# Optimization experiments

Hardware: AMD Instinct MI355X
Metric: run time of the kernel (lower is better)

Reference implementation:

```python
import jax, jax.numpy as jnp
import numpy as np

ENC_DIM, DEC_DIM, JOINT_DIM, VOCAB = 512, 640, 512, 1024
B, T, U = 8, 256, 64


def setup_inputs() -> dict:
    key = jax.random.key(0)
    ks = jax.random.split(key, 8)
    s_enc = 1.0 / np.sqrt(ENC_DIM)
    s_dec = 1.0 / np.sqrt(DEC_DIM)
    s_out = 1.0 / np.sqrt(2 * JOINT_DIM)
    return {
        "enc_out": jax.random.normal(ks[0], (B, T, ENC_DIM), jnp.float32),
        "pred_out": jax.random.normal(ks[1], (B, U, DEC_DIM), jnp.float32),
        "W_enc": jax.random.uniform(ks[2], (JOINT_DIM, ENC_DIM), jnp.float32, -s_enc, s_enc),
        "b_enc": jax.random.uniform(ks[3], (JOINT_DIM,), jnp.float32, -s_enc, s_enc),
        "W_pred": jax.random.uniform(ks[4], (JOINT_DIM, DEC_DIM), jnp.float32, -s_dec, s_dec),
        "b_pred": jax.random.uniform(ks[5], (JOINT_DIM,), jnp.float32, -s_dec, s_dec),
        "W_out": jax.random.uniform(ks[6], (VOCAB, 2 * JOINT_DIM), jnp.float32, -s_out, s_out),
        "b_out": jax.random.uniform(ks[7], (VOCAB,), jnp.float32, -s_out, s_out),
    }


def reference(enc_out, pred_out, W_enc, b_enc, W_pred, b_pred, W_out, b_out):
    # Dropout is identity in eval mode. fc_out on cat([enc_exp, pred_exp]) is
    # mathematically identical to splitting W_out in half and summing two
    # broadcast projections (avoids materializing the [B,T,U,2J] tensor).
    J = W_enc.shape[0]
    e = jnp.einsum('bte,je->btj', enc_out, W_enc) + b_enc    # [B,T,J]
    p = jnp.einsum('bud,jd->buj', pred_out, W_pred) + b_pred  # [B,U,J]
    W1, W2 = W_out[:, :J], W_out[:, J:]
    out = (jnp.einsum('btj,vj->btv', e, W1)[:, :, None, :]
           + jnp.einsum('buj,vj->buv', p, W2)[:, None, :, :]
           + b_out)                                           # [B,T,U,V]
    return out
```

## Files before the change

### kernel.cpp

```cpp
#include <hip/hip_runtime.h>

typedef float f4 __attribute__((ext_vector_type(4)));
typedef float f32x4 __attribute__((ext_vector_type(4)));
typedef short bf16x8 __attribute__((ext_vector_type(8)));
typedef unsigned short u16x8 __attribute__((ext_vector_type(8)));

static __device__ __forceinline__ unsigned short f2bf(float f) {
    unsigned int x = __builtin_bit_cast(unsigned int, f);
    x = (x + 0x7fffu + ((x >> 16) & 1u)) >> 16;
    return (unsigned short)x;
}
static __device__ __forceinline__ float bf2f(unsigned short h) {
    unsigned int x = ((unsigned int)h) << 16;
    return __builtin_bit_cast(float, x);
}

static __device__ __forceinline__ void gll16(const unsigned short* g, unsigned short* l) {
    __builtin_amdgcn_global_load_lds(
        (__attribute__((address_space(1))) void*)(g),
        (__attribute__((address_space(3))) void*)(l), 16, 0, 0);
}

static __device__ __forceinline__ int fragoff(int r, int s) {
    return r * 32 + ((s ^ ((r >> 1) & 3)) << 3);
}

struct GJobF {
    const float *A, *W;
    int lda, ldw;
    const float* bias;
    unsigned short *Ch, *Cl;
    int N, K, nbx;
};

__global__ __launch_bounds__(256, 3) void gemmcvt64(
    GJobF j0, GJobF j1, int nblk0, int nblk1,
    const float* __restrict__ Wo, unsigned short* __restrict__ Wo_h,
    unsigned short* __restrict__ Wo_l, int nWo8)
{
    __shared__ unsigned short lds[2][4][64 * 32];

    const int bid = blockIdx.x;
    const int tid = threadIdx.x;

    if (bid >= nblk0 + nblk1) {
        const int nblkc = (int)gridDim.x - nblk0 - nblk1;
        for (int g = (bid - nblk0 - nblk1) * 256 + tid; g < nWo8; g += nblkc * 256) {
            const int idx = g * 8;
            f4 a = *(const f4*)(Wo + idx);
            f4 b = *(const f4*)(Wo + idx + 4);
            u16x8 hv, lv;
            float s[8] = { a.x, a.y, a.z, a.w, b.x, b.y, b.z, b.w };
            #pragma unroll
            for (int i = 0; i < 8; ++i) {
                unsigned short h = f2bf(s[i]);
                hv[i] = h;
                lv[i] = f2bf(s[i] - bf2f(h));
            }
            *(u16x8*)(Wo_h + idx) = hv;
            *(u16x8*)(Wo_l + idx) = lv;
        }
        return;
    }

    const bool first = bid < nblk0;
    const GJobF J = first ? j0 : j1;
    const int local = first ? bid : bid - nblk0;
    const int m0 = (local % J.nbx) * 64;
    const int n0 = (local / J.nbx) * 64;

    const int lane = tid & 63;
    const int wid  = tid >> 6;
    const int wr   = wid >> 1, wc = wid & 1;
    const int lrow = lane & 15;
    const int s    = lane >> 4;

    const int row  = tid >> 2, slot = tid & 3;
    const int woff = fragoff(row, slot);
    const float* pA = J.A + (size_t)(m0 + row) * J.lda + slot * 8;
    const float* pW = J.W + (size_t)(n0 + row) * J.ldw + slot * 8;

    f4 ra0, ra1, rw0, rw1;

#define LOADREGS(k0) do { \
    ra0 = *(const f4*)(pA + (k0));     ra1 = *(const f4*)(pA + (k0) + 4); \
    rw0 = *(const f4*)(pW + (k0));     rw1 = *(const f4*)(pW + (k0) + 4); \
} while (0)

#define CVTWRITE(buf) do { \
    u16x8 ha, la, hw, lw; \
    float sa[8] = { ra0.x, ra0.y, ra0.z, ra0.w, ra1.x, ra1.y, ra1.z, ra1.w }; \
    float sw[8] = { rw0.x, rw0.y, rw0.z, rw0.w, rw1.x, rw1.y, rw1.z, rw1.w }; \
    _Pragma("unroll") \
    for (int i = 0; i < 8; ++i) { \
        unsigned short h = f2bf(sa[i]); \
        ha[i] = h; la[i] = f2bf(sa[i] - bf2f(h)); \
        h = f2bf(sw[i]); \
        hw[i] = h; lw[i] = f2bf(sw[i] - bf2f(h)); \
    } \
    *(u16x8*)&lds[buf][0][woff] = ha; \
    *(u16x8*)&lds[buf][1][woff] = la; \
    *(u16x8*)&lds[buf][2][woff] = hw; \
    *(u16x8*)&lds[buf][3][woff] = lw; \
} while (0)

    f32x4 acc[2][2];
    #pragma unroll
    for (int i = 0; i < 2; ++i)
        #pragma unroll
        for (int j = 0; j < 2; ++j) acc[i][j] = (f32x4){0.f, 0.f, 0.f, 0.f};

    const int nt = J.K / 32;

    LOADREGS(0);
    CVTWRITE(0);
    __syncthreads();

    int cur = 0;
    for (int t = 0; t < nt; ++t) {
        if (t + 1 < nt) LOADREGS((t + 1) * 32);

        bf16x8 ah[2], al[2], wh[2], wl[2];
        #pragma unroll
        for (int i = 0; i < 2; ++i) {
            const int ra = wr * 32 + i * 16 + lrow;
            const int rw = wc * 32 + i * 16 + lrow;
            ah[i] = *(const bf16x8*)&lds[cur][0][fragoff(ra, s)];
            al[i] = *(const bf16x8*)&lds[cur][1][fragoff(ra, s)];
            wh[i] = *(const bf16x8*)&lds[cur][2][fragoff(rw, s)];
            wl[i] = *(const bf16x8*)&lds[cur][3][fragoff(rw, s)];
        }
        #pragma unroll
        for (int i = 0; i < 2; ++i)
            #pragma unroll
            for (int j = 0; j < 2; ++j) {
                acc[i][j] = __builtin_amdgcn_mfma_f32_16x16x32_bf16(ah[i], wh[j], acc[i][j], 0, 0, 0);
                acc[i][j] = __builtin_amdgcn_mfma_f32_16x16x32_bf16(ah[i], wl[j], acc[i][j], 0, 0, 0);
                acc[i][j] = __builtin_amdgcn_mfma_f32_16x16x32_bf16(al[i], wh[j], acc[i][j], 0, 0, 0);
            }

        if (t + 1 < nt) {
            CVTWRITE(cur ^ 1);
            __syncthreads();
            cur ^= 1;
        }
    }
#undef LOADREGS
#undef CVTWRITE

    #pragma unroll
    for (int i = 0; i < 2; ++i) {
        const int rbase = m0 + wr * 32 + i * 16 + (lane >> 4) * 4;
        #pragma unroll
        for (int j = 0; j < 2; ++j) {
            const int col = n0 + wc * 32 + j * 16 + (lane & 15);
            const float bv = J.bias[col];
            #pragma unroll
            for (int r = 0; r < 4; ++r) {
                float v = acc[i][j][r] + bv;
                size_t off = (size_t)(rbase + r) * J.N + col;
                unsigned short h = f2bf(v);
                J.Ch[off] = h;
                J.Cl[off] = f2bf(v - bf2f(h));
            }
        }
    }
}

struct GJob {
    const unsigned short *Ah, *Al, *Wh, *Wl;
    int lda, ldw;
    const float* bias;
    float* Cf;
    int N, K, nbx;
};

__global__ __launch_bounds__(256, 3) void gemm64(GJob j0, GJob j1, int nblk0)
{
    __shared__ unsigned short lds[2][4][64 * 32];

    const bool first = (int)blockIdx.x < nblk0;
    const GJob J = first ? j0 : j1;
    const int local = first ? (int)blockIdx.x : (int)blockIdx.x - nblk0;
    const int m0 = (local % J.nbx) * 64;
    const int n0 = (local / J.nbx) * 64;

    const int tid  = threadIdx.x;
    const int lane = tid & 63;
    const int wid  = tid >> 6;
    const int wr   = wid >> 1, wc = wid & 1;
    const int lrow = lane & 15;
    const int s    = lane >> 4;

    const int srow  = wid * 16 + (lane >> 2);
    const int sslot = (lane & 3) ^ ((srow >> 1) & 3);
    const size_t gA = (size_t)(m0 + srow) * J.lda + sslot * 8;
    const size_t gW = (size_t)(n0 + srow) * J.ldw + sslot * 8;

    f32x4 acc[2][2];
    #pragma unroll
    for (int i = 0; i < 2; ++i)
        #pragma unroll
        for (int j = 0; j < 2; ++j) acc[i][j] = (f32x4){0.f, 0.f, 0.f, 0.f};

    const int nt = J.K / 32;

    gll16(J.Ah + gA, &lds[0][0][wid * 512]);
    gll16(J.Al + gA, &lds[0][1][wid * 512]);
    gll16(J.Wh + gW, &lds[0][2][wid * 512]);
    gll16(J.Wl + gW, &lds[0][3][wid * 512]);
    asm volatile("s_waitcnt vmcnt(0)" ::: "memory");
    __syncthreads();

    int cur = 0;
    for (int t = 0; t < nt; ++t) {
        if (t + 1 < nt) {
            const int k0 = (t + 1) * 32;
            gll16(J.Ah + gA + k0, &lds[cur ^ 1][0][wid * 512]);
            gll16(J.Al + gA + k0, &lds[cur ^ 1][1][wid * 512]);
            gll16(J.Wh + gW + k0, &lds[cur ^ 1][2][wid * 512]);
            gll16(J.Wl + gW + k0, &lds[cur ^ 1][3][wid * 512]);
        }

        bf16x8 ah[2], al[2], wh[2], wl[2];
        #pragma unroll
        for (int i = 0; i < 2; ++i) {
            const int ra = wr * 32 + i * 16 + lrow;
            const int rw = wc * 32 + i * 16 + lrow;
            ah[i] = *(const bf16x8*)&lds[cur][0][fragoff(ra, s)];
            al[i] = *(const bf16x8*)&lds[cur][1][fragoff(ra, s)];
            wh[i] = *(const bf16x8*)&lds[cur][2][fragoff(rw, s)];
            wl[i] = *(const bf16x8*)&lds[cur][3][fragoff(rw, s)];
        }
        #pragma unroll
        for (int i = 0; i < 2; ++i)
            #pragma unroll
            for (int j = 0; j < 2; ++j) {
                acc[i][j] = __builtin_amdgcn_mfma_f32_16x16x32_bf16(ah[i], wh[j], acc[i][j], 0, 0, 0);
                acc[i][j] = __builtin_amdgcn_mfma_f32_16x16x32_bf16(ah[i], wl[j], acc[i][j], 0, 0, 0);
                acc[i][j] = __builtin_amdgcn_mfma_f32_16x16x32_bf16(al[i], wh[j], acc[i][j], 0, 0, 0);
            }

        if (t + 1 < nt) {
            asm volatile("s_waitcnt vmcnt(0)" ::: "memory");
            __syncthreads();
            cur ^= 1;
        }
    }

    #pragma unroll
    for (int i = 0; i < 2; ++i) {
        const int rbase = m0 + wr * 32 + i * 16 + (lane >> 4) * 4;
        #pragma unroll
        for (int j = 0; j < 2; ++j) {
            const int col = n0 + wc * 32 + j * 16 + (lane & 15);
            const float bv = J.bias ? J.bias[col] : 0.f;
            #pragma unroll
            for (int r = 0; r < 4; ++r)
                J.Cf[(size_t)(rbase + r) * J.N + col] = acc[i][j][r] + bv;
        }
    }
}

__global__ __launch_bounds__(256) void bcast_kernel(
    const float* __restrict__ X, const float* __restrict__ Y,
    float* __restrict__ out, int T, int U)
{
    const int Vq  = 256;
    const int bt  = blockIdx.x;
    const int b   = bt / T;
    const int tid = threadIdx.x;

    const f4* X4 = (const f4*)X;
    const f4* Y4 = (const f4*)Y + (size_t)b * U * Vq;
    f4* O4 = (f4*)out + (size_t)bt * U * Vq;

    f4 x = X4[(size_t)bt * Vq + tid];
    #pragma unroll 4
    for (int u = 0; u < U; ++u) {
        f4 y = Y4[u * Vq + tid];
        f4 r = { x.x + y.x, x.y + y.y, x.z + y.z, x.w + y.w };
        __builtin_nontemporal_store(r, &O4[u * Vq + tid]);
    }
}

extern "C" void kernel_launch(void* const* d_in, const int* in_sizes, int n_in,
                              void* d_out, int out_size, void* d_ws, size_t ws_size,
                              hipStream_t stream) {
    (void)in_sizes; (void)n_in; (void)out_size; (void)ws_size;

    const int B = 8, T = 256, U = 64;
    const int ENC = 512, DEC = 640, J = 512, V = 1024;
    const int MT = B * T;
    const int MU = B * U;

    const float* enc    = (const float*)d_in[0];
    const float* pred   = (const float*)d_in[1];
    const float* W_enc  = (const float*)d_in[2];
    const float* b_enc  = (const float*)d_in[3];
    const float* W_pred = (const float*)d_in[4];
    const float* b_pred = (const float*)d_in[5];
    const float* W_out  = (const float*)d_in[6];
    const float* b_out  = (const float*)d_in[7];
    float* out = (float*)d_out;

    const int n_Wo = V * 2 * J;
    const int n_e  = MT * J;
    const int n_p  = MU * J;

    unsigned short* w = (unsigned short*)d_ws;
    unsigned short* Wo_h = w;
    unsigned short* Wo_l = Wo_h + n_Wo;
    unsigned short* e_h  = Wo_l + n_Wo;
    unsigned short* e_l  = e_h + n_e;
    unsigned short* p_h  = e_l + n_e;
    unsigned short* p_l  = p_h + n_p;
    float* ws_X = (float*)(p_l + n_p);
    float* ws_Y = ws_X + (size_t)MT * V;

    GJobF je = { enc,  W_enc,  ENC, ENC, b_enc,  e_h, e_l, J, ENC, MT / 64 };
    GJobF jp = { pred, W_pred, DEC, DEC, b_pred, p_h, p_l, J, DEC, MU / 64 };
    const int nbe = (MT / 64) * (J / 64);
    const int nbp = (MU / 64) * (J / 64);
    const int ncv = 64;
    gemmcvt64<<<nbe + nbp + ncv, 256, 0, stream>>>(
        je, jp, nbe, nbp, W_out, Wo_h, Wo_l, n_Wo / 8);

    GJob jx = { e_h, e_l, Wo_h, Wo_l, J, 2 * J, b_out, ws_X, V, J, MT / 64 };
    GJob jy = { p_h, p_l, Wo_h + J, Wo_l + J, J, 2 * J, nullptr, ws_Y, V, J, MU / 64 };
    const int nbx = (MT / 64) * (V / 64);
    const int nby = (MU / 64) * (V / 64);
    gemm64<<<nbx + nby, 256, 0, stream>>>(jx, jy, nbx);

    bcast_kernel<<<dim3(B * T), 256, 0, stream>>>(ws_X, ws_Y, out, T, U);
}
```

Before: 136.3 us.

## Deepen gemm64 load pipeline to four LDS stages and swizzle block order

Replaces the double-buffered K loop in gemm64 with a 4-buffer pipeline that keeps three tiles of global_load_lds in flight, using graded vmcnt waits and a single barrier per iteration instead of a full drain. It also remaps block indices so consecutive blocks are spread across eight groups, which changes L2 locality and XCD distribution. The larger LDS footprint lowers launch bounds occupancy from 3 to 2 blocks per CU. The GEMM stage is likely a small part of total time next to the broadcast output write.

```diff
diff --git a/kernel.cpp b/kernel.cpp
--- a/kernel.cpp
+++ b/kernel.cpp
@@ -175,13 +175,16 @@
     int N, K, nbx;
 };
 
-__global__ __launch_bounds__(256, 3) void gemm64(GJob j0, GJob j1, int nblk0)
+__global__ __launch_bounds__(256, 2) void gemm64(GJob j0, GJob j1, int nblk0)
 {
-    __shared__ unsigned short lds[2][4][64 * 32];
+    __shared__ unsigned short lds[4][4][64 * 32];
 
     const bool first = (int)blockIdx.x < nblk0;
     const GJob J = first ? j0 : j1;
-    const int local = first ? (int)blockIdx.x : (int)blockIdx.x - nblk0;
+    const int raw  = first ? (int)blockIdx.x : (int)blockIdx.x - nblk0;
+    const int nblk = first ? nblk0 : ((int)gridDim.x - nblk0);
+    const int q = nblk >> 3;
+    const int local = (raw & 7) * q + (raw >> 3);
     const int m0 = (local % J.nbx) * 64;
     const int n0 = (local / J.nbx) * 64;
 
@@ -197,6 +200,13 @@
     const size_t gA = (size_t)(m0 + srow) * J.lda + sslot * 8;
     const size_t gW = (size_t)(n0 + srow) * J.ldw + sslot * 8;
 
+#define STAGE(buf, k0) do { \
+    gll16(J.Ah + gA + (k0), &lds[buf][0][wid * 512]); \
+    gll16(J.Al + gA + (k0), &lds[buf][1][wid * 512]); \
+    gll16(J.Wh + gW + (k0), &lds[buf][2][wid * 512]); \
+    gll16(J.Wl + gW + (k0), &lds[buf][3][wid * 512]); \
+} while (0)
+
     f32x4 acc[2][2];
     #pragma unroll
     for (int i = 0; i < 2; ++i)
@@ -205,23 +215,21 @@
 
     const int nt = J.K / 32;
 
-    gll16(J.Ah + gA, &lds[0][0][wid * 512]);
-    gll16(J.Al + gA, &lds[0][1][wid * 512]);
-    gll16(J.Wh + gW, &lds[0][2][wid * 512]);
-    gll16(J.Wl + gW, &lds[0][3][wid * 512]);
-    asm volatile("s_waitcnt vmcnt(0)" ::: "memory");
-    __syncthreads();
-
-    int cur = 0;
+    STAGE(0, 0);
+    STAGE(1, 32);
+    STAGE(2, 64);
+
     for (int t = 0; t < nt; ++t) {
-        if (t + 1 < nt) {
-            const int k0 = (t + 1) * 32;
-            gll16(J.Ah + gA + k0, &lds[cur ^ 1][0][wid * 512]);
-            gll16(J.Al + gA + k0, &lds[cur ^ 1][1][wid * 512]);
-            gll16(J.Wh + gW + k0, &lds[cur ^ 1][2][wid * 512]);
-            gll16(J.Wl + gW + k0, &lds[cur ^ 1][3][wid * 512]);
-        }
-
+        if (t < nt - 2)      asm volatile("s_waitcnt vmcnt(8)" ::: "memory");
+        else if (t == nt - 2) asm volatile("s_waitcnt vmcnt(4)" ::: "memory");
+        else                  asm volatile("s_waitcnt vmcnt(0)" ::: "memory");
+        __builtin_amdgcn_sched_barrier(0);
+        __builtin_amdgcn_s_barrier();
+        __builtin_amdgcn_sched_barrier(0);
+
+        if (t + 3 < nt) STAGE((t + 3) & 3, (t + 3) * 32);
+
+        const int cur = t & 3;
         bf16x8 ah[2], al[2], wh[2], wl[2];
         #pragma unroll
         for (int i = 0; i < 2; ++i) {
@@ -240,13 +248,8 @@
                 acc[i][j] = __builtin_amdgcn_mfma_f32_16x16x32_bf16(ah[i], wl[j], acc[i][j], 0, 0, 0);
                 acc[i][j] = __builtin_amdgcn_mfma_f32_16x16x32_bf16(al[i], wh[j], acc[i][j], 0, 0, 0);
             }
-
-        if (t + 1 < nt) {
-            asm volatile("s_waitcnt vmcnt(0)" ::: "memory");
-            __syncthreads();
-            cur ^= 1;
-        }
-    }
+    }
+#undef STAGE
 
     #pragma unroll
     for (int i = 0; i < 2; ++i) {
```

Measured after the change: 139.0 us. 1.02x slower.

## Fuse three kernels into persistent work-queue kernel with dependency flags

Applied to the files above, without the earlier changes.

Replaces the three separate launches (projection GEMMs with W_out conversion, output-vocab GEMMs, broadcast add) with one persistent kernel. Blocks pull jobs from an atomic counter and wait on per-panel/per-row-block flags through acquire/release atomics. Dependent stages can then start as soon as their inputs are ready instead of waiting at kernel boundaries. The cost is spin-waiting with sleeps, an extra flag-zeroing launch, and lower occupancy hint (2 blocks per CU).

```diff
diff --git a/kernel.cpp b/kernel.cpp
--- a/kernel.cpp
+++ b/kernel.cpp
@@ -25,50 +25,46 @@
     return r * 32 + ((s ^ ((r >> 1) & 3)) << 3);
 }
 
-struct GJobF {
-    const float *A, *W;
-    int lda, ldw;
-    const float* bias;
-    unsigned short *Ch, *Cl;
-    int N, K, nbx;
-};
-
-__global__ __launch_bounds__(256, 3) void gemmcvt64(
-    GJobF j0, GJobF j1, int nblk0, int nblk1,
+static __device__ __forceinline__ void flag_wait(int* f, int target) {
+    while (__hip_atomic_load(f, __ATOMIC_ACQUIRE, __HIP_MEMORY_SCOPE_AGENT) < target)
+        __builtin_amdgcn_s_sleep(16);
+}
+static __device__ __forceinline__ void flag_bump(int* f, int tid) {
+    __syncthreads();
+    if (tid == 0)
+        __hip_atomic_fetch_add(f, 1, __ATOMIC_RELEASE, __HIP_MEMORY_SCOPE_AGENT);
+}
+
+
+static __device__ __forceinline__ void cvt_panel(
     const float* __restrict__ Wo, unsigned short* __restrict__ Wo_h,
-    unsigned short* __restrict__ Wo_l, int nWo8)
-{
-    __shared__ unsigned short lds[2][4][64 * 32];
-
-    const int bid = blockIdx.x;
-    const int tid = threadIdx.x;
-
-    if (bid >= nblk0 + nblk1) {
-        const int nblkc = (int)gridDim.x - nblk0 - nblk1;
-        for (int g = (bid - nblk0 - nblk1) * 256 + tid; g < nWo8; g += nblkc * 256) {
-            const int idx = g * 8;
-            f4 a = *(const f4*)(Wo + idx);
-            f4 b = *(const f4*)(Wo + idx + 4);
-            u16x8 hv, lv;
-            float s[8] = { a.x, a.y, a.z, a.w, b.x, b.y, b.z, b.w };
-            #pragma unroll
-            for (int i = 0; i < 8; ++i) {
-                unsigned short h = f2bf(s[i]);
-                hv[i] = h;
-                lv[i] = f2bf(s[i] - bf2f(h));
-            }
-            *(u16x8*)(Wo_h + idx) = hv;
-            *(u16x8*)(Wo_l + idx) = lv;
-        }
-        return;
-    }
-
-    const bool first = bid < nblk0;
-    const GJobF J = first ? j0 : j1;
-    const int local = first ? bid : bid - nblk0;
-    const int m0 = (local % J.nbx) * 64;
-    const int n0 = (local / J.nbx) * 64;
-
+    unsigned short* __restrict__ Wo_l, int c, int tid)
+{
+    const int base = c * 8192;
+    for (int g = tid; g < 8192; g += 256) {
+        const int idx = (base + g) * 8;
+        f4 a = *(const f4*)(Wo + idx);
+        f4 b = *(const f4*)(Wo + idx + 4);
+        u16x8 hv, lv;
+        float s[8] = { a.x, a.y, a.z, a.w, b.x, b.y, b.z, b.w };
+        #pragma unroll
+        for (int i = 0; i < 8; ++i) {
+            unsigned short h = f2bf(s[i]);
+            hv[i] = h;
+            lv[i] = f2bf(s[i] - bf2f(h));
+        }
+        *(u16x8*)(Wo_h + idx) = hv;
+        *(u16x8*)(Wo_l + idx) = lv;
+    }
+}
+
+static __device__ __forceinline__ void gemm_cvt_tile(
+    unsigned short* lds,
+    const float* __restrict__ A, const float* __restrict__ W,
+    int lda, int ldw, int K, const float* __restrict__ bias,
+    unsigned short* __restrict__ Ch, unsigned short* __restrict__ Cl,
+    int N, int m0, int n0, int tid)
+{
     const int lane = tid & 63;
     const int wid  = tid >> 6;
     const int wr   = wid >> 1, wc = wid & 1;
@@ -77,8 +73,8 @@
 
     const int row  = tid >> 2, slot = tid & 3;
     const int woff = fragoff(row, slot);
-    const float* pA = J.A + (size_t)(m0 + row) * J.lda + slot * 8;
-    const float* pW = J.W + (size_t)(n0 + row) * J.ldw + slot * 8;
+    const float* pA = A + (size_t)(m0 + row) * lda + slot * 8;
+    const float* pW = W + (size_t)(n0 + row) * ldw + slot * 8;
 
     f4 ra0, ra1, rw0, rw1;
 
@@ -98,10 +94,10 @@
         h = f2bf(sw[i]); \
         hw[i] = h; lw[i] = f2bf(sw[i] - bf2f(h)); \
     } \
-    *(u16x8*)&lds[buf][0][woff] = ha; \
-    *(u16x8*)&lds[buf][1][woff] = la; \
-    *(u16x8*)&lds[buf][2][woff] = hw; \
-    *(u16x8*)&lds[buf][3][woff] = lw; \
+    *(u16x8*)&lds[((buf) * 4 + 0) * 2048 + woff] = ha; \
+    *(u16x8*)&lds[((buf) * 4 + 1) * 2048 + woff] = la; \
+    *(u16x8*)&lds[((buf) * 4 + 2) * 2048 + woff] = hw; \
+    *(u16x8*)&lds[((buf) * 4 + 3) * 2048 + woff] = lw; \
 } while (0)
 
     f32x4 acc[2][2];
@@ -110,7 +106,7 @@
         #pragma unroll
         for (int j = 0; j < 2; ++j) acc[i][j] = (f32x4){0.f, 0.f, 0.f, 0.f};
 
-    const int nt = J.K / 32;
+    const int nt = K / 32;
 
     LOADREGS(0);
     CVTWRITE(0);
@@ -125,10 +121,10 @@
         for (int i = 0; i < 2; ++i) {
             const int ra = wr * 32 + i * 16 + lrow;
             const int rw = wc * 32 + i * 16 + lrow;
-            ah[i] = *(const bf16x8*)&lds[cur][0][fragoff(ra, s)];
-            al[i] = *(const bf16x8*)&lds[cur][1][fragoff(ra, s)];
-            wh[i] = *(const bf16x8*)&lds[cur][2][fragoff(rw, s)];
-            wl[i] = *(const bf16x8*)&lds[cur][3][fragoff(rw, s)];
+            ah[i] = *(const bf16x8*)&lds[(cur * 4 + 0) * 2048 + fragoff(ra, s)];
+            al[i] = *(const bf16x8*)&lds[(cur * 4 + 1) * 2048 + fragoff(ra, s)];
+            wh[i] = *(const bf16x8*)&lds[(cur * 4 + 2) * 2048 + fragoff(rw, s)];
+            wl[i] = *(const bf16x8*)&lds[(cur * 4 + 3) * 2048 + fragoff(rw, s)];
         }
         #pragma unroll
         for (int i = 0; i < 2; ++i)
@@ -154,38 +150,26 @@
         #pragma unroll
         for (int j = 0; j < 2; ++j) {
             const int col = n0 + wc * 32 + j * 16 + (lane & 15);
-            const float bv = J.bias[col];
+            const float bv = bias[col];
             #pragma unroll
             for (int r = 0; r < 4; ++r) {
                 float v = acc[i][j][r] + bv;
-                size_t off = (size_t)(rbase + r) * J.N + col;
+                size_t off = (size_t)(rbase + r) * N + col;
                 unsigned short h = f2bf(v);
-                J.Ch[off] = h;
-                J.Cl[off] = f2bf(v - bf2f(h));
+                Ch[off] = h;
+                Cl[off] = f2bf(v - bf2f(h));
             }
         }
     }
 }
 
-struct GJob {
-    const unsigned short *Ah, *Al, *Wh, *Wl;
-    int lda, ldw;
-    const float* bias;
-    float* Cf;
-    int N, K, nbx;
-};
-
-__global__ __launch_bounds__(256, 3) void gemm64(GJob j0, GJob j1, int nblk0)
-{
-    __shared__ unsigned short lds[2][4][64 * 32];
-
-    const bool first = (int)blockIdx.x < nblk0;
-    const GJob J = first ? j0 : j1;
-    const int local = first ? (int)blockIdx.x : (int)blockIdx.x - nblk0;
-    const int m0 = (local % J.nbx) * 64;
-    const int n0 = (local / J.nbx) * 64;
-
-    const int tid  = threadIdx.x;
+static __device__ __forceinline__ void gemm_plane_tile(
+    unsigned short* lds,
+    const unsigned short* __restrict__ Ah, const unsigned short* __restrict__ Al,
+    const unsigned short* __restrict__ Wh, const unsigned short* __restrict__ Wl,
+    int lda, int ldw, int K, const float* __restrict__ bias,
+    float* __restrict__ Cf, int N, int m0, int n0, int tid)
+{
     const int lane = tid & 63;
     const int wid  = tid >> 6;
     const int wr   = wid >> 1, wc = wid & 1;
@@ -194,8 +178,15 @@
 
     const int srow  = wid * 16 + (lane >> 2);
     const int sslot = (lane & 3) ^ ((srow >> 1) & 3);
-    const size_t gA = (size_t)(m0 + srow) * J.lda + sslot * 8;
-    const size_t gW = (size_t)(n0 + srow) * J.ldw + sslot * 8;
+    const size_t gA = (size_t)(m0 + srow) * lda + sslot * 8;
+    const size_t gW = (size_t)(n0 + srow) * ldw + sslot * 8;
+
+#define STAGE(buf, k0) do { \
+    gll16(Ah + gA + (k0), &lds[((buf) * 4 + 0) * 2048 + wid * 512]); \
+    gll16(Al + gA + (k0), &lds[((buf) * 4 + 1) * 2048 + wid * 512]); \
+    gll16(Wh + gW + (k0), &lds[((buf) * 4 + 2) * 2048 + wid * 512]); \
+    gll16(Wl + gW + (k0), &lds[((buf) * 4 + 3) * 2048 + wid * 512]); \
+} while (0)
 
     f32x4 acc[2][2];
     #pragma unroll
@@ -203,34 +194,25 @@
         #pragma unroll
         for (int j = 0; j < 2; ++j) acc[i][j] = (f32x4){0.f, 0.f, 0.f, 0.f};
 
-    const int nt = J.K / 32;
-
-    gll16(J.Ah + gA, &lds[0][0][wid * 512]);
-    gll16(J.Al + gA, &lds[0][1][wid * 512]);
-    gll16(J.Wh + gW, &lds[0][2][wid * 512]);
-    gll16(J.Wl + gW, &lds[0][3][wid * 512]);
+    const int nt = K / 32;
+
+    STAGE(0, 0);
     asm volatile("s_waitcnt vmcnt(0)" ::: "memory");
     __syncthreads();
 
     int cur = 0;
     for (int t = 0; t < nt; ++t) {
-        if (t + 1 < nt) {
-            const int k0 = (t + 1) * 32;
-            gll16(J.Ah + gA + k0, &lds[cur ^ 1][0][wid * 512]);
-            gll16(J.Al + gA + k0, &lds[cur ^ 1][1][wid * 512]);
-            gll16(J.Wh + gW + k0, &lds[cur ^ 1][2][wid * 512]);
-            gll16(J.Wl + gW + k0, &lds[cur ^ 1][3][wid * 512]);
-        }
+        if (t + 1 < nt) STAGE(cur ^ 1, (t + 1) * 32);
 
         bf16x8 ah[2], al[2], wh[2], wl[2];
         #pragma unroll
         for (int i = 0; i < 2; ++i) {
             const int ra = wr * 32 + i * 16 + lrow;
             const int rw = wc * 32 + i * 16 + lrow;
-            ah[i] = *(const bf16x8*)&lds[cur][0][fragoff(ra, s)];
-            al[i] = *(const bf16x8*)&lds[cur][1][fragoff(ra, s)];
-            wh[i] = *(const bf16x8*)&lds[cur][2][fragoff(rw, s)];
-            wl[i] = *(const bf16x8*)&lds[cur][3][fragoff(rw, s)];
+            ah[i] = *(const bf16x8*)&lds[(cur * 4 + 0) * 2048 + fragoff(ra, s)];
+            al[i] = *(const bf16x8*)&lds[(cur * 4 + 1) * 2048 + fragoff(ra, s)];
+            wh[i] = *(const bf16x8*)&lds[(cur * 4 + 2) * 2048 + fragoff(rw, s)];
+            wl[i] = *(const bf16x8*)&lds[(cur * 4 + 3) * 2048 + fragoff(rw, s)];
         }
         #pragma unroll
         for (int i = 0; i < 2; ++i)
@@ -247,6 +229,7 @@
             cur ^= 1;
         }
     }
+#undef STAGE
 
     #pragma unroll
     for (int i = 0; i < 2; ++i) {
@@ -254,33 +237,100 @@
         #pragma unroll
         for (int j = 0; j < 2; ++j) {
             const int col = n0 + wc * 32 + j * 16 + (lane & 15);
-            const float bv = J.bias ? J.bias[col] : 0.f;
+            const float bv = bias ? bias[col] : 0.f;
             #pragma unroll
             for (int r = 0; r < 4; ++r)
-                J.Cf[(size_t)(rbase + r) * J.N + col] = acc[i][j][r] + bv;
-        }
-    }
-}
-
-__global__ __launch_bounds__(256) void bcast_kernel(
+                Cf[(size_t)(rbase + r) * N + col] = acc[i][j][r] + bv;
+        }
+    }
+}
+
+static __device__ __forceinline__ void bcast_row(
     const float* __restrict__ X, const float* __restrict__ Y,
-    float* __restrict__ out, int T, int U)
-{
-    const int Vq  = 256;
-    const int bt  = blockIdx.x;
-    const int b   = bt / T;
-    const int tid = threadIdx.x;
-
+    float* __restrict__ out, int bt, int tid)
+{
+    const int Vq = 256;
+    const int b  = bt >> 8;
     const f4* X4 = (const f4*)X;
-    const f4* Y4 = (const f4*)Y + (size_t)b * U * Vq;
-    f4* O4 = (f4*)out + (size_t)bt * U * Vq;
+    const f4* Y4 = (const f4*)Y + (size_t)b * 64 * Vq;
+    f4* O4 = (f4*)out + (size_t)bt * 64 * Vq;
 
     f4 x = X4[(size_t)bt * Vq + tid];
     #pragma unroll 4
-    for (int u = 0; u < U; ++u) {
+    for (int u = 0; u < 64; ++u) {
         f4 y = Y4[u * Vq + tid];
         f4 r = { x.x + y.x, x.y + y.y, x.z + y.z, x.w + y.w };
         __builtin_nontemporal_store(r, &O4[u * Vq + tid]);
+    }
+}
+
+__global__ __launch_bounds__(128) void zero_flags(int* flags, int n) {
+    if ((int)threadIdx.x < n) flags[threadIdx.x] = 0;
+}
+
+__global__ __launch_bounds__(256, 2) void joiner_fused(
+    const float* __restrict__ enc, const float* __restrict__ pred,
+    const float* __restrict__ W_enc, const float* __restrict__ b_enc,
+    const float* __restrict__ W_pred, const float* __restrict__ b_pred,
+    const float* __restrict__ W_out, const float* __restrict__ b_out,
+    unsigned short* Wo_h, unsigned short* Wo_l,
+    unsigned short* e_h, unsigned short* e_l,
+    unsigned short* p_h, unsigned short* p_l,
+    float* ws_X, float* ws_Y, float* out, int* flags)
+{
+    __shared__ unsigned short lds[2 * 4 * 2048];
+    __shared__ int s_job;
+    const int tid = threadIdx.x;
+
+    int* job_ctr = flags + 0;
+    int* wo_f = flags + 1;
+    int* p_f  = flags + 17;
+    int* e_f  = flags + 25;
+    int* y_f  = flags + 57;
+    int* x_f  = flags + 58;
+
+    for (;;) {
+        __syncthreads();
+        if (tid == 0) s_job = atomicAdd(job_ctr, 1);
+        __syncthreads();
+        const int job = s_job;
+        if (job >= 3024) return;
+
+        if (job < 16) {
+            cvt_panel(W_out, Wo_h, Wo_l, job, tid);
+            flag_bump(&wo_f[job], tid);
+        } else if (job < 80) {
+            const int jl = job - 16, m = jl >> 3, n = jl & 7;
+            gemm_cvt_tile(lds, pred, W_pred, 640, 640, 640, b_pred,
+                          p_h, p_l, 512, m * 64, n * 64, tid);
+            flag_bump(&p_f[m], tid);
+        } else if (job < 336) {
+            const int jl = job - 80, m = jl >> 3, n = jl & 7;
+            gemm_cvt_tile(lds, enc, W_enc, 512, 512, 512, b_enc,
+                          e_h, e_l, 512, m * 64, n * 64, tid);
+            flag_bump(&e_f[m], tid);
+        } else if (job < 464) {
+            const int jl = job - 336, n = jl >> 3, m = jl & 7;
+            flag_wait(&p_f[m], 8);
+            flag_wait(&wo_f[n], 1);
+            gemm_plane_tile(lds, p_h, p_l, Wo_h + 512, Wo_l + 512,
+                            512, 1024, 512, nullptr, ws_Y, 1024,
+                            m * 64, n * 64, tid);
+            flag_bump(y_f, tid);
+        } else if (job < 976) {
+            const int jl = job - 464, m = jl >> 4, n = jl & 15;
+            flag_wait(&e_f[m], 8);
+            flag_wait(&wo_f[n], 1);
+            gemm_plane_tile(lds, e_h, e_l, Wo_h, Wo_l,
+                            512, 1024, 512, b_out, ws_X, 1024,
+                            m * 64, n * 64, tid);
+            flag_bump(&x_f[m], tid);
+        } else {
+            const int bt = job - 976;
+            flag_wait(&x_f[bt >> 6], 16);
+            flag_wait(y_f, 128);
+            bcast_row(ws_X, ws_Y, out, bt, tid);
+        }
     }
 }
 
@@ -290,7 +340,7 @@
     (void)in_sizes; (void)n_in; (void)out_size; (void)ws_size;
 
     const int B = 8, T = 256, U = 64;
-    const int ENC = 512, DEC = 640, J = 512, V = 1024;
+    const int J = 512, V = 1024;
     const int MT = B * T;
     const int MU = B * U;
 
@@ -317,20 +367,10 @@
     unsigned short* p_l  = p_h + n_p;
     float* ws_X = (float*)(p_l + n_p);
     float* ws_Y = ws_X + (size_t)MT * V;
-
-    GJobF je = { enc,  W_enc,  ENC, ENC, b_enc,  e_h, e_l, J, ENC, MT / 64 };
-    GJobF jp = { pred, W_pred, DEC, DEC, b_pred, p_h, p_l, J, DEC, MU / 64 };
-    const int nbe = (MT / 64) * (J / 64);
-    const int nbp = (MU / 64) * (J / 64);
-    const int ncv = 64;
-    gemmcvt64<<<nbe + nbp + ncv, 256, 0, stream>>>(
-        je, jp, nbe, nbp, W_out, Wo_h, Wo_l, n_Wo / 8);
-
-    GJob jx = { e_h, e_l, Wo_h, Wo_l, J, 2 * J, b_out, ws_X, V, J, MT / 64 };
-    GJob jy = { p_h, p_l, Wo_h + J, Wo_l + J, J, 2 * J, nullptr, ws_Y, V, J, MU / 64 };
-    const int nbx = (MT / 64) * (V / 64);
-    const int nby = (MU / 64) * (V / 64);
-    gemm64<<<nbx + nby, 256, 0, stream>>>(jx, jy, nbx);
-
-    bcast_kernel<<<dim3(B * T), 256, 0, stream>>>(ws_X, ws_Y, out, T, U);
-}
+    int*   flags = (int*)(ws_Y + (size_t)MU * V);
+
+    zero_flags<<<1, 128, 0, stream>>>(flags, 90);
+    joiner_fused<<<512, 256, 0, stream>>>(
+        enc, pred, W_enc, b_enc, W_pred, b_pred, W_out, b_out,
+        Wo_h, Wo_l, e_h, e_l, p_h, p_l, ws_X, ws_Y, out, flags);
+}
```

Result: slower. 437.4 us (+220.9%).

## Fuse encoder-side output GEMM into broadcast-add kernel

Applied to the files above, without the earlier changes.

Removes the separate X GEMM and its workspace round trip by computing 8 rows of e·W1+b_out per block with MFMA directly from global memory, staging them in LDS, then streaming the broadcast add with Y. The Y GEMM now runs alone. The cost is that every block rereads the full W1 hi/lo from global memory without LDS tiling, and it uses only half of each 16-row MFMA tile.

```diff
diff --git a/kernel.cpp b/kernel.cpp
--- a/kernel.cpp
+++ b/kernel.cpp
@@ -175,13 +175,11 @@
     int N, K, nbx;
 };
 
-__global__ __launch_bounds__(256, 3) void gemm64(GJob j0, GJob j1, int nblk0)
+__global__ __launch_bounds__(256, 3) void gemm64(GJob J)
 {
     __shared__ unsigned short lds[2][4][64 * 32];
 
-    const bool first = (int)blockIdx.x < nblk0;
-    const GJob J = first ? j0 : j1;
-    const int local = first ? (int)blockIdx.x : (int)blockIdx.x - nblk0;
+    const int local = blockIdx.x;
     const int m0 = (local % J.nbx) * 64;
     const int n0 = (local / J.nbx) * 64;
 
@@ -254,33 +252,76 @@
         #pragma unroll
         for (int j = 0; j < 2; ++j) {
             const int col = n0 + wc * 32 + j * 16 + (lane & 15);
-            const float bv = J.bias ? J.bias[col] : 0.f;
             #pragma unroll
             for (int r = 0; r < 4; ++r)
-                J.Cf[(size_t)(rbase + r) * J.N + col] = acc[i][j][r] + bv;
-        }
-    }
-}
-
-__global__ __launch_bounds__(256) void bcast_kernel(
-    const float* __restrict__ X, const float* __restrict__ Y,
-    float* __restrict__ out, int T, int U)
+                J.Cf[(size_t)(rbase + r) * J.N + col] = acc[i][j][r];
+        }
+    }
+}
+
+__global__ __launch_bounds__(256) void fused_xb(
+    const unsigned short* __restrict__ e_h, const unsigned short* __restrict__ e_l,
+    const unsigned short* __restrict__ W1h, const unsigned short* __restrict__ W1l,
+    const float* __restrict__ b_out,
+    const float* __restrict__ Y,
+    float* __restrict__ out)
 {
-    const int Vq  = 256;
-    const int bt  = blockIdx.x;
-    const int b   = bt / T;
-    const int tid = threadIdx.x;
-
-    const f4* X4 = (const f4*)X;
-    const f4* Y4 = (const f4*)Y + (size_t)b * U * Vq;
-    f4* O4 = (f4*)out + (size_t)bt * U * Vq;
-
-    f4 x = X4[(size_t)bt * Vq + tid];
-    #pragma unroll 4
-    for (int u = 0; u < U; ++u) {
-        f4 y = Y4[u * Vq + tid];
-        f4 r = { x.x + y.x, x.y + y.y, x.z + y.z, x.w + y.w };
-        __builtin_nontemporal_store(r, &O4[u * Vq + tid]);
+    __shared__ float Xs[8][1024];
+
+    const int tid  = threadIdx.x;
+    const int lane = tid & 63;
+    const int wid  = tid >> 6;
+    const int bt0  = blockIdx.x * 8;
+    const int b    = bt0 >> 8;
+    const int nb   = wid * 256;
+
+    const int arow = bt0 + ((lane & 15) & 7);
+    const int koff = (lane >> 4) * 8;
+    const unsigned short* pAh = e_h + (size_t)arow * 512 + koff;
+    const unsigned short* pAl = e_l + (size_t)arow * 512 + koff;
+
+    f32x4 acc[16];
+    #pragma unroll
+    for (int i = 0; i < 16; ++i) acc[i] = (f32x4){0.f, 0.f, 0.f, 0.f};
+
+    for (int k0 = 0; k0 < 512; k0 += 32) {
+        bf16x8 ah = *(const bf16x8*)(pAh + k0);
+        bf16x8 al = *(const bf16x8*)(pAl + k0);
+        #pragma unroll
+        for (int nt = 0; nt < 16; ++nt) {
+            const size_t wrow = (size_t)(nb + nt * 16 + (lane & 15)) * 1024 + k0 + koff;
+            bf16x8 wh = *(const bf16x8*)(W1h + wrow);
+            bf16x8 wl = *(const bf16x8*)(W1l + wrow);
+            acc[nt] = __builtin_amdgcn_mfma_f32_16x16x32_bf16(ah, wh, acc[nt], 0, 0, 0);
+            acc[nt] = __builtin_amdgcn_mfma_f32_16x16x32_bf16(ah, wl, acc[nt], 0, 0, 0);
+            acc[nt] = __builtin_amdgcn_mfma_f32_16x16x32_bf16(al, wh, acc[nt], 0, 0, 0);
+        }
+    }
+
+    const int r0 = (lane >> 4) * 4;
+    #pragma unroll
+    for (int nt = 0; nt < 16; ++nt) {
+        const int col = nb + nt * 16 + (lane & 15);
+        const float bv = b_out[col];
+        if (r0 < 8) {
+            #pragma unroll
+            for (int r = 0; r < 4; ++r)
+                Xs[r0 + r][col] = acc[nt][r] + bv;
+        }
+    }
+    __syncthreads();
+
+    const f4* Y4 = (const f4*)Y + (size_t)b * 64 * 256;
+    f4* O4 = (f4*)out + (size_t)bt0 * 64 * 256;
+    for (int btl = 0; btl < 8; ++btl) {
+        f4 x = *(const f4*)&Xs[btl][tid * 4];
+        f4* rowp = O4 + (size_t)btl * 64 * 256;
+        #pragma unroll 4
+        for (int u = 0; u < 64; ++u) {
+            f4 y = Y4[u * 256 + tid];
+            f4 r = { x.x + y.x, x.y + y.y, x.z + y.z, x.w + y.w };
+            __builtin_nontemporal_store(r, &rowp[u * 256 + tid]);
+        }
     }
 }
 
@@ -315,8 +356,7 @@
     unsigned short* e_l  = e_h + n_e;
     unsigned short* p_h  = e_l + n_e;
     unsigned short* p_l  = p_h + n_p;
-    float* ws_X = (float*)(p_l + n_p);
-    float* ws_Y = ws_X + (size_t)MT * V;
+    float* ws_Y = (float*)(p_l + n_p);
 
     GJobF je = { enc,  W_enc,  ENC, ENC, b_enc,  e_h, e_l, J, ENC, MT / 64 };
     GJobF jp = { pred, W_pred, DEC, DEC, b_pred, p_h, p_l, J, DEC, MU / 64 };
@@ -326,11 +366,10 @@
     gemmcvt64<<<nbe + nbp + ncv, 256, 0, stream>>>(
         je, jp, nbe, nbp, W_out, Wo_h, Wo_l, n_Wo / 8);
 
-    GJob jx = { e_h, e_l, Wo_h, Wo_l, J, 2 * J, b_out, ws_X, V, J, MT / 64 };
     GJob jy = { p_h, p_l, Wo_h + J, Wo_l + J, J, 2 * J, nullptr, ws_Y, V, J, MU / 64 };
-    const int nbx = (MT / 64) * (V / 64);
     const int nby = (MU / 64) * (V / 64);
-    gemm64<<<nbx + nby, 256, 0, stream>>>(jx, jy, nbx);
-
-    bcast_kernel<<<dim3(B * T), 256, 0, stream>>>(ws_X, ws_Y, out, T, U);
-}
+    gemm64<<<nby, 256, 0, stream>>>(jy);
+
+    fused_xb<<<MT / 8, 256, 0, stream>>>(
+        e_h, e_l, Wo_h, Wo_l, b_out, ws_Y, out);
+}
```

Measured after the change: 216.2 us. 58.7% more time.
